# Kernel optimization log

Measured on AMD Instinct MI355X. Metric: run time of the kernel, lower is better.

Reference implementation:

```python
import jax, jax.numpy as jnp
import numpy as np

B, D, H, L = 2, 1024, 16, 4
BLK = 16                 # block_size == max_text_tokens
MT, MF = 16, 2032        # max_text_tokens, max_font_tokens
S = MT + MF              # 2048
NB = S // BLK            # 128 blocks
V = 490                  # font_vocab_size
HD = D // H              # 64
WIN = 30                 # 3*max_glyph_tokens/block_size = 3*160/16
NGLOB, NRAND = 1, 2      # BigBird global / random blocks
SOS = 0.42


def _make_layout():
    # Deterministic BigBird block layout per head: [H, NB, NB] bool
    rng = np.random.default_rng(0)
    layout = np.zeros((H, NB, NB), dtype=bool)
    layout[:, :NGLOB, :] = True          # global rows
    layout[:, :, :NGLOB] = True          # global cols
    for i in range(NB):                  # sliding window
        layout[:, i, max(0, i - WIN // 2):min(NB, i + WIN // 2 + 1)] = True
    for h in range(H):                   # random blocks
        for i in range(NB):
            layout[h, i, rng.choice(NB, size=NRAND, replace=False)] = True
    return jnp.asarray(layout)


def setup_inputs() -> dict:
    key = jax.random.key(0)
    ks = jax.random.split(key, 16)
    p = lambda k, shape: (0.02 * jax.random.normal(k, shape)).astype(jnp.float32)
    return {
        "text_embeddings": jax.random.normal(ks[0], (B, MT, D), jnp.float32),
        "font_embeddings": jax.random.normal(ks[1], (B, MF, D), jnp.float32),
        "layout": _make_layout(),
        "Wq": p(ks[2], (L, D, D)), "bq": jnp.zeros((L, D), jnp.float32),
        "Wk": p(ks[3], (L, D, D)), "bk": jnp.zeros((L, D), jnp.float32),
        "Wv": p(ks[4], (L, D, D)), "bv": jnp.zeros((L, D), jnp.float32),
        "Wo": p(ks[5], (L, D, D)), "bo": jnp.zeros((L, D), jnp.float32),
        "ln1_g": jnp.ones((L, D), jnp.float32), "ln1_b": jnp.zeros((L, D), jnp.float32),
        "ln2_g": jnp.ones((L, D), jnp.float32), "ln2_b": jnp.zeros((L, D), jnp.float32),
        "W1": p(ks[6], (L, D, 4 * D)), "b1": jnp.zeros((L, 4 * D), jnp.float32),
        "W2": p(ks[7], (L, 4 * D, D)), "b2": jnp.zeros((L, D), jnp.float32),
        "lnf_g": jnp.ones((D,), jnp.float32), "lnf_b": jnp.zeros((D,), jnp.float32),
        "Wout": p(ks[8], (D, V)),
    }


def _ln(x, g, b, eps=1e-5):
    mu = x.mean(-1, keepdims=True)
    var = ((x - mu) ** 2).mean(-1, keepdims=True)
    return (x - mu) * jax.lax.rsqrt(var + eps) * g + b


def _forward(text_embeddings, font_embeddings, layout, Wq, bq, Wk, bk, Wv, bv, Wo, bo,
             ln1_g, ln1_b, ln2_g, ln2_b, W1, b1, W2, b2, lnf_g, lnf_b, Wout):
    sos = jnp.full((B, 1, D), SOS, text_embeddings.dtype)
    x = jnp.concatenate([sos, text_embeddings, font_embeddings[:, :-1, :]], axis=1)  # [B,S,D]
    # token-level mask = block-sparse BigBird layout AND causal -> [H,S,S]
    tok_mask = jnp.repeat(jnp.repeat(layout, BLK, axis=1), BLK, axis=2)
    tok_mask = tok_mask & jnp.tril(jnp.ones((S, S), bool))[None]
    neg = jnp.asarray(-1e9, x.dtype)
    scale = jnp.asarray(1.0 / np.sqrt(HD), x.dtype)

    def layer(x, p):
        wq, bq_, wk, bk_, wv, bv_, wo, bo_, g1, gb1, g2, gb2, w1, bb1, w2, bb2 = p
        q = (x @ wq + bq_).reshape(B, S, H, HD).transpose(0, 2, 1, 3)
        k = (x @ wk + bk_).reshape(B, S, H, HD).transpose(0, 2, 1, 3)
        v = (x @ wv + bv_).reshape(B, S, H, HD).transpose(0, 2, 1, 3)
        scores = jnp.einsum('bhqd,bhkd->bhqk', q, k) * scale
        scores = jnp.where(tok_mask[None], scores, neg)
        probs = jax.nn.softmax(scores, axis=-1)
        a = jnp.einsum('bhqk,bhkd->bhqd', probs, v).transpose(0, 2, 1, 3).reshape(B, S, D)
        a = a @ wo + bo_
        x = _ln(x + a, g1, gb1)                                   # post-norm residual
        m = jax.nn.gelu(x @ w1 + bb1, approximate=False) @ w2 + bb2  # dropout=eval no-op
        x = _ln(x + m, g2, gb2)
        return x, None

    params = (Wq, bq, Wk, bk, Wv, bv, Wo, bo, ln1_g, ln1_b, ln2_g, ln2_b, W1, b1, W2, b2)
    x, _ = jax.lax.scan(jax.checkpoint(layer), x, params)
    logits = _ln(x, lnf_g, lnf_b) @ Wout                          # [B,S,V]
    return logits[:, :MT, :], logits[:, MT:, :]


def reference(text_embeddings, font_embeddings, layout, Wq, bq, Wk, bk, Wv, bv, Wo, bo,
              ln1_g, ln1_b, ln2_g, ln2_b, W1, b1, W2, b2, lnf_g, lnf_b, Wout):
    return _forward(text_embeddings, font_embeddings, layout, Wq, bq, Wk, bk, Wv, bv, Wo, bo,
                    ln1_g, ln1_b, ln2_g, ln2_b, W1, b1, W2, b2, lnf_g, lnf_b, Wout)
```

## Files before the change

kernel.cpp:

```cpp
#include <hip/hip_runtime.h>
#include <hip/hip_bf16.h>
#include <math.h>


typedef __hip_bfloat16 bf16;
typedef __attribute__((ext_vector_type(8))) short bf16x8;
typedef __attribute__((ext_vector_type(8))) unsigned short us8;
typedef __attribute__((ext_vector_type(4))) unsigned short us4;
typedef __attribute__((ext_vector_type(4))) float f32x4;
typedef __attribute__((ext_vector_type(8))) _Float16 f16x8;

#define S_LEN 2048
#define D_MODEL 1024
#define NBLK 128
#define NHEAD 16
#define BATCH 2
#define M_ROWS 4096
#define VOCAB 490

__device__ __forceinline__ float ldw(const void* p, size_t i, bool bf) {
    return bf ? __bfloat162float(((const bf16*)p)[i]) : ((const float*)p)[i];
}
__device__ __forceinline__ bool is_bf(const unsigned* probe) {
    return probe[0] != 0x3F800000u;
}
__device__ __forceinline__ unsigned short f2b(float f) {
    union { float f; unsigned u; } x; x.f = f;
    return (unsigned short)((x.u + 0x7FFFu + ((x.u >> 16) & 1u)) >> 16);
}
__device__ __forceinline__ unsigned short f2h(float f) {
    union { _Float16 h; unsigned short u; } x; x.h = (_Float16)f;
    return x.u;
}
__device__ __forceinline__ unsigned packh(float a, float b) {
    return (unsigned)f2h(a) | ((unsigned)f2h(b) << 16);
}

__global__ __launch_bounds__(256) void norm_layout_kernel(
    const unsigned char* __restrict__ lraw, unsigned char* __restrict__ mask)
{
    int i = blockIdx.x * 256 + threadIdx.x;
    bool bytes_mode = (lraw[1] == 1);
    unsigned char v;
    if (bytes_mode) v = lraw[i] ? 1 : 0;
    else            v = ((const unsigned*)lraw)[i] ? 1 : 0;
    mask[i] = v;
}

__global__ __launch_bounds__(256) void build_x_kernel(
    const void* __restrict__ text, const void* __restrict__ font,
    float* __restrict__ x, unsigned short* __restrict__ xb,
    const unsigned* __restrict__ probe)
{
    bool bf = is_bf(probe);
    size_t idx = (size_t)blockIdx.x * 256 + threadIdx.x;
    int d = (int)(idx & 1023);
    int s = (int)((idx >> 10) & 2047);
    int b = (int)(idx >> 21);
    float v;
    if (s == 0)       v = bf ? 0.419921875f : 0.42f;
    else if (s <= 16) v = ldw(text, ((size_t)(b * 16 + (s - 1))) * 1024 + d, bf);
    else              v = ldw(font, ((size_t)(b * 2032 + (s - 17))) * 1024 + d, bf);
    x[idx] = v;
    xb[idx] = f2b(v);
}

__global__ __launch_bounds__(256) void transw_kernel(
    const void* __restrict__ W, size_t wOff, unsigned short* __restrict__ Wt,
    int K, int N, const unsigned* __restrict__ probe)
{
    bool bf = is_bf(probe);
    __shared__ unsigned short tile[32][34];
    int k0 = blockIdx.x * 32, n0 = blockIdx.y * 32;
    int t = threadIdx.x, c = t & 31, r0 = t >> 5;
    #pragma unroll
    for (int i = 0; i < 4; ++i) {
        int n = n0 + c;
        float v = (n < N) ? ldw(W, wOff + (size_t)(k0 + r0 + i * 8) * N + n, bf) : 0.f;
        tile[r0 + i * 8][c] = f2b(v);
    }
    __syncthreads();
    #pragma unroll
    for (int i = 0; i < 4; ++i)
        Wt[(size_t)(n0 + r0 + i * 8) * K + k0 + c] = tile[c][r0 + i * 8];
}

__global__ __launch_bounds__(256) void transw4_kernel(
    const void* __restrict__ Wa, const void* __restrict__ Wb,
    const void* __restrict__ Wc, const void* __restrict__ Wd,
    size_t wOff, unsigned short* __restrict__ wt,
    const unsigned* __restrict__ probe)
{
    bool bf = is_bf(probe);
    int z = blockIdx.z;
    const void* W = z == 0 ? Wa : (z == 1 ? Wb : (z == 2 ? Wc : Wd));
    unsigned short* Wt = wt + (size_t)z * (1u << 20);
    __shared__ unsigned short tile[32][34];
    int k0 = blockIdx.x * 32, n0 = blockIdx.y * 32;
    int t = threadIdx.x, c = t & 31, r0 = t >> 5;
    #pragma unroll
    for (int i = 0; i < 4; ++i) {
        float v = ldw(W, wOff + (size_t)(k0 + r0 + i * 8) * 1024 + n0 + c, bf);
        tile[r0 + i * 8][c] = f2b(v);
    }
    __syncthreads();
    #pragma unroll
    for (int i = 0; i < 4; ++i)
        Wt[(size_t)(n0 + r0 + i * 8) * 1024 + k0 + c] = tile[c][r0 + i * 8];
}

__global__ __launch_bounds__(512) void gemm_kernel(
    const unsigned short* __restrict__ Ab,
    const unsigned short* __restrict__ Wt, size_t wtStride,
    const void* __restrict__ b0, const void* __restrict__ b1p, const void* __restrict__ b2p,
    size_t bOff,
    float* __restrict__ C0, float* __restrict__ C1, float* __restrict__ C2,
    void* __restrict__ Cb0, void* __restrict__ Cb1, void* __restrict__ Cb2,
    float* __restrict__ Cp,
    int M, int N, int K, int act, int outmode, const unsigned* __restrict__ probe)
{
    bool bf = is_bf(probe);
    __shared__ __align__(16) unsigned short As[2][128 * 64];
    __shared__ __align__(16) unsigned short Bs[2][128 * 64];

    int t    = threadIdx.x;
    int lane = t & 63;
    int wid  = t >> 6;
    int wm   = wid >> 2;
    int wn   = wid & 3;

    int gx  = gridDim.x;
    int nwg = gx * gridDim.y;
    int bid = blockIdx.y * gx + blockIdx.x;
    int swz = (bid & 7) * (nwg >> 3) + (bid >> 3);
    int m0  = (swz / gx) * 128;
    int n0t = (swz % gx) * 128;
    int sel = n0t / N;
    int n0  = n0t - sel * N;
    int zz  = blockIdx.z;
    int Kit = K / gridDim.z;
    int kbase = zz * Kit;

    const void* bias = sel == 0 ? b0 : (sel == 1 ? b1p : b2p);
    float* C         = sel == 0 ? C0 : (sel == 1 ? C1 : C2);
    void* Cb         = sel == 0 ? Cb0 : (sel == 1 ? Cb1 : Cb2);
    const unsigned short* Wtb = Wt + (size_t)sel * wtStride;
    const bool vtr = (outmode == 3 && sel == 2);

    f32x4 acc[4][2];
    #pragma unroll
    for (int i = 0; i < 4; i++)
        #pragma unroll
        for (int j = 0; j < 2; j++)
            acc[i][j] = (f32x4){0.f, 0.f, 0.f, 0.f};

    const int fm = lane & 15;

    auto stageA = [&](int bb, int kt) {
        int k0 = kbase + (kt << 6);
        #pragma unroll
        for (int c = 0; c < 2; ++c) {
            int p    = (wid * 2 + c) * 64 + lane;
            int row  = p >> 3;
            int cp   = p & 7;
            int csrc = cp ^ (row & 7);
            const unsigned short* src = Ab + (size_t)(m0 + row) * K + k0 + csrc * 8;
            unsigned short* dst = &As[bb][(wid * 2 + c) * 512];
            __builtin_amdgcn_global_load_lds(
                (const __attribute__((address_space(1))) unsigned int*)src,
                (__attribute__((address_space(3))) unsigned int*)dst, 16, 0, 0);
        }
    };
    auto stageB = [&](int bb, int kt) {
        int k0 = kbase + (kt << 6);
        #pragma unroll
        for (int c = 0; c < 2; ++c) {
            int p    = (wid * 2 + c) * 64 + lane;
            int row  = p >> 3;
            int cp   = p & 7;
            int csrc = cp ^ (row & 7);
            const unsigned short* src = Wtb + (size_t)(n0 + row) * K + k0 + csrc * 8;
            unsigned short* dst = &Bs[bb][(wid * 2 + c) * 512];
            __builtin_amdgcn_global_load_lds(
                (const __attribute__((address_space(1))) unsigned int*)src,
                (__attribute__((address_space(3))) unsigned int*)dst, 16, 0, 0);
        }
    };
    auto compute = [&](int bb) {
        #pragma unroll
        for (int kk = 0; kk < 2; ++kk) {
            int cq = kk * 4 + (lane >> 4);
            bf16x8 af[4], bfr[2];
            #pragma unroll
            for (int i = 0; i < 4; ++i) {
                int r = wm * 64 + i * 16 + fm;
                af[i] = *(const bf16x8*)(&As[bb][r * 64 + (cq ^ (r & 7)) * 8]);
            }
            #pragma unroll
            for (int j = 0; j < 2; ++j) {
                int n = wn * 32 + j * 16 + fm;
                bfr[j] = *(const bf16x8*)(&Bs[bb][n * 64 + (cq ^ (n & 7)) * 8]);
            }
            #pragma unroll
            for (int i = 0; i < 4; ++i)
                #pragma unroll
                for (int j = 0; j < 2; ++j)
                    acc[i][j] = __builtin_amdgcn_mfma_f32_16x16x32_bf16(
                        af[i], bfr[j], acc[i][j], 0, 0, 0);
        }
    };

    int nt = Kit >> 6;
    stageA(0, 0);
    stageB(0, 0);
    __syncthreads();

    for (int kt = 0; kt < nt; ++kt) {
        int cur = kt & 1;
        bool more = (kt + 1) < nt;
        if (more) { stageA(cur ^ 1, kt + 1); stageB(cur ^ 1, kt + 1); }
        compute(cur);
        __syncthreads();
    }

    int rq = (lane >> 4) * 4;
    #pragma unroll
    for (int j = 0; j < 2; ++j) {
        int n = n0 + wn * 32 + j * 16 + fm;
        if (n >= N) continue;
        float bv = (bias && zz == 0) ? ldw(bias, bOff + n, bf) : 0.f;
        #pragma unroll
        for (int i = 0; i < 4; ++i) {
            int mb = m0 + wm * 64 + i * 16 + rq;
            if (zz > 0) {
                #pragma unroll
                for (int r = 0; r < 4; ++r)
                    Cp[(size_t)(mb + r) * N + n] = acc[i][j][r];
                continue;
            }
            if (vtr) {
                us4 o;
                #pragma unroll
                for (int r = 0; r < 4; ++r) o[r] = f2h(acc[i][j][r] + bv);
                int bb2 = mb >> 11, s0 = mb & 2047, hh = n >> 6, dd = n & 63;
                *(us4*)(&((unsigned short*)Cb)[((((size_t)(bb2 * 16 + hh)) * 64 + dd) << 11) + s0]) = o;
                continue;
            }
            #pragma unroll
            for (int r = 0; r < 4; ++r) {
                int m = mb + r;
                float v = acc[i][j][r] + bv;
                if (act == 1) v = 0.5f * v * (1.f + erff(v * 0.70710678118654752f));
                if (outmode == 0) {
                    C[(size_t)m * N + n] = v;
                } else if (outmode == 2) {
                    ((unsigned short*)Cb)[(size_t)m * N + n] = f2b(v);
                } else if (outmode == 3) {
                    ((unsigned short*)Cb)[(size_t)m * N + n] = f2h(v);
                } else {
                    int b = m >> 11;
                    int s = m & 2047;
                    size_t dst;
                    if (s < 16) dst = ((size_t)(b * 16 + s)) * N + n;
                    else        dst = (size_t)(BATCH * 16) * N + ((size_t)(b * 2032 + (s - 16))) * N + n;
                    if (bf) ((unsigned short*)Cb)[dst] = f2b(v);
                    else    ((float*)Cb)[dst] = v;
                }
            }
        }
    }
}

__global__ __launch_bounds__(256) void attn_kernel(
    const unsigned short* __restrict__ q16, const unsigned short* __restrict__ k16,
    const unsigned short* __restrict__ v16t, const unsigned char* __restrict__ mask,
    unsigned short* __restrict__ ab)
{
    int qgrp = blockIdx.x;
    int h = blockIdx.y, b = blockIdx.z;

    __shared__ __align__(16) unsigned short ksd[64 * 64];
    __shared__ __align__(16) unsigned short vst[64 * 64];
    __shared__ unsigned char cflag[33];
    __shared__ unsigned char aclist[33];
    __shared__ int nac;

    int t = threadIdx.x, lane = t & 63, w = t >> 6;
    int qb = qgrp * 4 + w;
    const int fm = lane & 15, rq = lane >> 4;

    const unsigned char* mrow0 = mask + ((size_t)h * NBLK) * NBLK;

    if (t <= qgrp) {
        int jc = t;
        bool f = false;
        #pragma unroll
        for (int mb = 0; mb < 4; ++mb) {
            int j = jc * 4 + mb;
            #pragma unroll
            for (int ww = 0; ww < 4; ++ww) {
                int qq = qgrp * 4 + ww;
                f = f || ((j <= qq) && mrow0[qq * NBLK + j]);
            }
        }
        cflag[jc] = f ? 1 : 0;
    }
    __syncthreads();
    if (t == 0) {
        int n = 0;
        for (int jc = 0; jc <= qgrp; ++jc)
            if (cflag[jc]) aclist[n++] = (unsigned char)jc;
        nac = n;
    }

    int qrow = qb * 16 + fm;
    size_t qbase = ((size_t)(b * S_LEN + qrow)) * D_MODEL + h * 64;
    f16x8 qf0 = *(const f16x8*)(q16 + qbase + rq * 8);
    f16x8 qf1 = *(const f16x8*)(q16 + qbase + 32 + rq * 8);

    f32x4 O[4];
    #pragma unroll
    for (int c = 0; c < 4; ++c) O[c] = (f32x4){0.f, 0.f, 0.f, 0.f};
    float m_run = -1e30f, l_run = 0.f;
    const f16x8 hzero = (f16x8){0,0,0,0,0,0,0,0};

    __syncthreads();
    int nacl = nac;

    const int srow = t >> 2;
    const int sg   = (t & 3) * 2;
    const size_t vtbase = ((size_t)(b * NHEAD + h) * 64) * S_LEN;
    us8 kr0, kr1, vr0, vr1;

    auto loadKV = [&](int jc) {
        size_t kb = ((size_t)(b * S_LEN + jc * 64 + srow)) * D_MODEL + h * 64 + sg * 8;
        kr0 = *(const us8*)(k16 + kb);
        kr1 = *(const us8*)(k16 + kb + 8);
        size_t vb_ = vtbase + (size_t)srow * S_LEN + jc * 64 + sg * 8;
        vr0 = *(const us8*)(v16t + vb_);
        vr1 = *(const us8*)(v16t + vb_ + 8);
    };
    auto writeKV = [&]() {
        int p0 = (sg) ^ (srow & 7), p1 = (sg + 1) ^ (srow & 7);
        *(us8*)(&ksd[srow * 64 + p0 * 8]) = kr0;
        *(us8*)(&ksd[srow * 64 + p1 * 8]) = kr1;
        *(us8*)(&vst[srow * 64 + p0 * 8]) = vr0;
        *(us8*)(&vst[srow * 64 + p1 * 8]) = vr1;
    };

    if (nacl > 0) loadKV(aclist[0]);

    for (int ci = 0; ci < nacl; ++ci) {
        int jc = aclist[ci];
        __syncthreads();
        writeKV();
        if (ci + 1 < nacl) loadKV(aclist[ci + 1]);
        __syncthreads();

        #pragma unroll
        for (int mb = 0; mb < 4; ++mb) {
            int j = jc * 4 + mb;
            bool actv = (j <= qb) && mrow0[qb * NBLK + j];
            if (!actv) continue;

            int krow = mb * 16 + fm;
            f16x8 kf0 = *(const f16x8*)(&ksd[krow * 64 + ((0 * 4 + rq) ^ (krow & 7)) * 8]);
            f16x8 kf1 = *(const f16x8*)(&ksd[krow * 64 + ((1 * 4 + rq) ^ (krow & 7)) * 8]);
            f32x4 st = (f32x4){0.f, 0.f, 0.f, 0.f};
            st = __builtin_amdgcn_mfma_f32_16x16x32_f16(kf0, qf0, st, 0, 0, 0);
            st = __builtin_amdgcn_mfma_f32_16x16x32_f16(kf1, qf1, st, 0, 0, 0);

            float s[4];
            #pragma unroll
            for (int r = 0; r < 4; ++r) {
                s[r] = st[r] * 0.125f;
                if (j == qb && (rq * 4 + r) > fm) s[r] = -1e30f;
            }
            float mx = fmaxf(fmaxf(s[0], s[1]), fmaxf(s[2], s[3]));
            mx = fmaxf(mx, __shfl_xor(mx, 16));
            mx = fmaxf(mx, __shfl_xor(mx, 32));
            mx = fmaxf(m_run, mx);
            float al = expf(m_run - mx);
            float p[4]; float ls = 0.f;
            #pragma unroll
            for (int r = 0; r < 4; ++r) {
                p[r] = (s[r] < -1e29f) ? 0.f : expf(s[r] - mx);
                ls += p[r];
            }
            ls += __shfl_xor(ls, 16);
            ls += __shfl_xor(ls, 32);
            l_run = l_run * al + ls;
            m_run = mx;

            unsigned ph01 = packh(p[0], p[1]), ph23 = packh(p[2], p[3]);
            int s0 = fm + (((rq & 1) * 2) << 4);
            int s1 = s0 + 16;
            unsigned w0 = __shfl(ph01, s0), w1 = __shfl(ph23, s0);
            unsigned w2 = __shfl(ph01, s1), w3 = __shfl(ph23, s1);
            union { unsigned u[4]; f16x8 v; } pcv;
            pcv.u[0] = w0; pcv.u[1] = w1; pcv.u[2] = w2; pcv.u[3] = w3;
            f16x8 pa = (rq < 2) ? pcv.v : hzero;

            float al0 = __shfl(al, rq * 4 + 0), al1 = __shfl(al, rq * 4 + 1);
            float al2 = __shfl(al, rq * 4 + 2), al3 = __shfl(al, rq * 4 + 3);
            #pragma unroll
            for (int c = 0; c < 4; ++c) {
                O[c][0] *= al0; O[c][1] *= al1; O[c][2] *= al2; O[c][3] *= al3;
                f16x8 vb = hzero;
                if (rq < 2) {
                    int vrow = c * 16 + fm;
                    vb = *(const f16x8*)(&vst[vrow * 64 + ((mb * 2 + rq) ^ (vrow & 7)) * 8]);
                }
                O[c] = __builtin_amdgcn_mfma_f32_16x16x32_f16(pa, vb, O[c], 0, 0, 0);
            }
        }
    }

    float li0 = 1.f / __shfl(l_run, rq * 4 + 0);
    float li1 = 1.f / __shfl(l_run, rq * 4 + 1);
    float li2 = 1.f / __shfl(l_run, rq * 4 + 2);
    float li3 = 1.f / __shfl(l_run, rq * 4 + 3);
    size_t obase = ((size_t)(b * S_LEN + qb * 16)) * D_MODEL + h * 64;
    #pragma unroll
    for (int c = 0; c < 4; ++c) {
        ab[obase + (size_t)(rq * 4 + 0) * D_MODEL + c * 16 + fm] = f2b(O[c][0] * li0);
        ab[obase + (size_t)(rq * 4 + 1) * D_MODEL + c * 16 + fm] = f2b(O[c][1] * li1);
        ab[obase + (size_t)(rq * 4 + 2) * D_MODEL + c * 16 + fm] = f2b(O[c][2] * li2);
        ab[obase + (size_t)(rq * 4 + 3) * D_MODEL + c * 16 + fm] = f2b(O[c][3] * li3);
    }
}

__global__ __launch_bounds__(256) void add_ln_kernel(
    const float* __restrict__ xin, const float* __restrict__ res,
    const float* __restrict__ res2,
    float* __restrict__ xout, unsigned short* __restrict__ bfout,
    const void* __restrict__ g, size_t gOff,
    const void* __restrict__ bt, size_t bOff, const unsigned* __restrict__ probe)
{
    bool bf = is_bf(probe);
    int row = blockIdx.x;
    int t = threadIdx.x;
    __shared__ float red[4];

    float4 xv = ((const float4*)(xin + (size_t)row * D_MODEL))[t];
    if (res) {
        float4 rv = ((const float4*)(res + (size_t)row * D_MODEL))[t];
        xv.x += rv.x; xv.y += rv.y; xv.z += rv.z; xv.w += rv.w;
    }
    if (res2) {
        float4 rv = ((const float4*)(res2 + (size_t)row * D_MODEL))[t];
        xv.x += rv.x; xv.y += rv.y; xv.z += rv.z; xv.w += rv.w;
    }
    float s = xv.x + xv.y + xv.z + xv.w;
    for (int off = 32; off > 0; off >>= 1) s += __shfl_down(s, off);
    if ((t & 63) == 0) red[t >> 6] = s;
    __syncthreads();
    float mu = (red[0] + red[1] + red[2] + red[3]) * (1.f / 1024.f);
    __syncthreads();

    float d0 = xv.x - mu, d1 = xv.y - mu, d2 = xv.z - mu, d3 = xv.w - mu;
    float s2 = d0 * d0 + d1 * d1 + d2 * d2 + d3 * d3;
    for (int off = 32; off > 0; off >>= 1) s2 += __shfl_down(s2, off);
    if ((t & 63) == 0) red[t >> 6] = s2;
    __syncthreads();
    float var = (red[0] + red[1] + red[2] + red[3]) * (1.f / 1024.f);
    float rstd = rsqrtf(var + 1e-5f);

    int dbase = t * 4;
    float4 ov;
    ov.x = d0 * rstd * ldw(g, gOff + dbase + 0, bf) + ldw(bt, bOff + dbase + 0, bf);
    ov.y = d1 * rstd * ldw(g, gOff + dbase + 1, bf) + ldw(bt, bOff + dbase + 1, bf);
    ov.z = d2 * rstd * ldw(g, gOff + dbase + 2, bf) + ldw(bt, bOff + dbase + 2, bf);
    ov.w = d3 * rstd * ldw(g, gOff + dbase + 3, bf) + ldw(bt, bOff + dbase + 3, bf);
    ((float4*)(xout + (size_t)row * D_MODEL))[t] = ov;
    if (bfout) {
        us4 bv = { f2b(ov.x), f2b(ov.y), f2b(ov.z), f2b(ov.w) };
        *(us4*)(bfout + (size_t)row * D_MODEL + dbase) = bv;
    }
}

extern "C" void kernel_launch(void* const* d_in, const int* in_sizes, int n_in,
                              void* d_out, int out_size, void* d_ws, size_t ws_size,
                              hipStream_t stream) {
    const void* text  = d_in[0];
    const void* font  = d_in[1];
    const unsigned char* lraw = (const unsigned char*)d_in[2];
    const void* Wq    = d_in[3];
    const void* bq    = d_in[4];
    const void* Wk    = d_in[5];
    const void* bk    = d_in[6];
    const void* Wv    = d_in[7];
    const void* bv    = d_in[8];
    const void* Wo    = d_in[9];
    const void* bo_   = d_in[10];
    const void* ln1g  = d_in[11];
    const void* ln1b  = d_in[12];
    const void* ln2g  = d_in[13];
    const void* ln2b  = d_in[14];
    const void* W1    = d_in[15];
    const void* b1    = d_in[16];
    const void* W2    = d_in[17];
    const void* b2    = d_in[18];
    const void* lnfg  = d_in[19];
    const void* lnfb  = d_in[20];
    const void* Wout  = d_in[21];
    const unsigned* probe = (const unsigned*)d_in[11];

    const size_t Q = (size_t)M_ROWS * D_MODEL;
    float* ws = (float*)d_ws;
    float* x  = ws;
    float* G0 = ws + Q;
    unsigned short* q16 = (unsigned short*)(ws + 2 * Q);
    unsigned short* k16 = q16 + Q;
    unsigned short* v16 = k16 + Q;
    unsigned short* hb  = (unsigned short*)(ws + 2 * Q);
    unsigned short* xb  = (unsigned short*)(ws + 4 * Q);
    unsigned short* ab  = (unsigned short*)(ws + 4 * Q + Q / 2);
    unsigned char* mask = (unsigned char*)(ws + 5 * Q);
    unsigned short* wt  = (unsigned short*)((char*)d_ws + 5 * Q * 4 + 262144);

    const size_t baseEnd = 5 * Q * 4 + 262144 + 8 * ((size_t)1 << 20) * 2;
    bool canSplit = ws_size >= baseEnd + Q * 4;
    float* part = (float*)((char*)d_ws + baseEnd);

    norm_layout_kernel<<<(NHEAD * NBLK * NBLK) / 256, 256, 0, stream>>>(lraw, mask);
    build_x_kernel<<<(BATCH * S_LEN * D_MODEL) / 256, 256, 0, stream>>>(text, font, x, xb, probe);

    dim3 gQKV(3 * D_MODEL / 128, M_ROWS / 128);
    dim3 gD(D_MODEL / 128, M_ROWS / 128, canSplit ? 2 : 1);
    dim3 gF(4 * D_MODEL / 128, M_ROWS / 128);
    dim3 gV((VOCAB + 127) / 128, M_ROWS / 128);

    const size_t MSZ = (size_t)1 << 20;
    const float* r2 = canSplit ? part : nullptr;

    for (int l = 0; l < 4; l++) {
        size_t wo  = (size_t)l * D_MODEL * D_MODEL;
        size_t bo1 = (size_t)l * D_MODEL;
        size_t w1o = (size_t)l * D_MODEL * 4 * D_MODEL;
        size_t b1o = (size_t)l * 4 * D_MODEL;

        transw4_kernel<<<dim3(32, 32, 4), 256, 0, stream>>>(Wq, Wk, Wv, Wo, wo, wt, probe);

        gemm_kernel<<<gQKV, 512, 0, stream>>>(xb, wt, MSZ, bq, bk, bv, bo1,
                                              nullptr, nullptr, nullptr, q16, k16, v16,
                                              nullptr,
                                              M_ROWS, D_MODEL, D_MODEL, 0, 3, probe);
        attn_kernel<<<dim3(S_LEN / 64, NHEAD, BATCH), 256, 0, stream>>>(
            q16, k16, v16, mask, ab);
        gemm_kernel<<<gD, 512, 0, stream>>>(ab, wt + 3 * MSZ, 0, bo_, bo_, bo_, bo1,
                                            G0, G0, G0, nullptr, nullptr, nullptr,
                                            part,
                                            M_ROWS, D_MODEL, D_MODEL, 0, 0, probe);
        add_ln_kernel<<<M_ROWS, 256, 0, stream>>>(x, G0, r2, x, xb, ln1g, bo1, ln1b, bo1, probe);

        transw_kernel<<<dim3(32, 128), 256, 0, stream>>>(W1, w1o, wt, D_MODEL, 4 * D_MODEL, probe);
        transw_kernel<<<dim3(128, 32), 256, 0, stream>>>(W2, w1o, wt + 4 * MSZ, 4 * D_MODEL, D_MODEL, probe);

        gemm_kernel<<<gF, 512, 0, stream>>>(xb, wt, 0, b1, b1, b1, b1o,
                                            nullptr, nullptr, nullptr, hb, hb, hb,
                                            nullptr,
                                            M_ROWS, 4 * D_MODEL, D_MODEL, 1, 2, probe);
        gemm_kernel<<<gD, 512, 0, stream>>>(hb, wt + 4 * MSZ, 0, b2, b2, b2, bo1,
                                            G0, G0, G0, nullptr, nullptr, nullptr,
                                            part,
                                            M_ROWS, D_MODEL, 4 * D_MODEL, 0, 0, probe);
        add_ln_kernel<<<M_ROWS, 256, 0, stream>>>(x, G0, r2, x, xb, ln2g, bo1, ln2b, bo1, probe);
    }

    add_ln_kernel<<<M_ROWS, 256, 0, stream>>>(x, nullptr, nullptr, G0, ab, lnfg, 0, lnfb, 0, probe);
    transw_kernel<<<dim3(32, 16), 256, 0, stream>>>(Wout, 0, wt, D_MODEL, VOCAB, probe);
    gemm_kernel<<<gV, 512, 0, stream>>>(ab, wt, 0, nullptr, nullptr, nullptr, 0,
                                        nullptr, nullptr, nullptr, d_out, d_out, d_out,
                                        nullptr,
                                        M_ROWS, VOCAB, D_MODEL, 0, 1, probe);
}
```

Measured before the change: 1.332 ms.

## Vectorize weight transposes, use polynomial GELU, reverse attention block order

The weight transpose kernels now read and write four elements per thread with vector loads and stores, and the shared tile is padded to 36 columns. The exact erff in the GELU epilogue is replaced by an Abramowitz-Stegun polynomial using a fast reciprocal and __expf, which lowers accuracy to about 1e-7 absolute error in erf. The attention grid processes query groups in reverse order so the heavier late blocks with more active key columns are scheduled first. These are separate ideas that each target conversion bandwidth, epilogue math cost, or load balance.

Measured after the change: 1.309 ms. Within noise of the previous version (-1.7%).

```diff
diff --git a/kernel.cpp b/kernel.cpp
--- a/kernel.cpp
+++ b/kernel.cpp
@@ -34,6 +34,15 @@
 }
 __device__ __forceinline__ unsigned packh(float a, float b) {
     return (unsigned)f2h(a) | ((unsigned)f2h(b) << 16);
+}
+__device__ __forceinline__ float gelu_exact(float v) {
+    float z = fabsf(v) * 0.70710678118654752f;
+    float t = __builtin_amdgcn_rcpf(fmaf(0.3275911f, z, 1.f));
+    float p = t * fmaf(t, fmaf(t, fmaf(t, fmaf(t, 1.061405429f, -1.453152027f),
+                  1.421413741f), -0.284496736f), 0.254829592f);
+    float er = 1.f - p * __expf(-z * z);
+    er = copysignf(er, v);
+    return 0.5f * v * (1.f + er);
 }
 
 __global__ __launch_bounds__(256) void norm_layout_kernel(
@@ -70,19 +79,32 @@
     int K, int N, const unsigned* __restrict__ probe)
 {
     bool bf = is_bf(probe);
-    __shared__ unsigned short tile[32][34];
+    __shared__ unsigned short tile[32][36];
     int k0 = blockIdx.x * 32, n0 = blockIdx.y * 32;
-    int t = threadIdx.x, c = t & 31, r0 = t >> 5;
-    #pragma unroll
-    for (int i = 0; i < 4; ++i) {
-        int n = n0 + c;
-        float v = (n < N) ? ldw(W, wOff + (size_t)(k0 + r0 + i * 8) * N + n, bf) : 0.f;
-        tile[r0 + i * 8][c] = f2b(v);
-    }
-    __syncthreads();
-    #pragma unroll
-    for (int i = 0; i < 4; ++i)
-        Wt[(size_t)(n0 + r0 + i * 8) * K + k0 + c] = tile[c][r0 + i * 8];
+    int t = threadIdx.x;
+    int r  = t >> 3;
+    int c4 = (t & 7) * 4;
+    int n = n0 + c4;
+    us4 tv;
+    if (n + 4 <= N) {
+        if (bf) {
+            tv = *(const us4*)((const unsigned short*)W + wOff + (size_t)(k0 + r) * N + n);
+        } else {
+            float4 f = *(const float4*)((const float*)W + wOff + (size_t)(k0 + r) * N + n);
+            tv = (us4){ f2b(f.x), f2b(f.y), f2b(f.z), f2b(f.w) };
+        }
+    } else {
+        #pragma unroll
+        for (int i = 0; i < 4; ++i)
+            tv[i] = (n + i < N) ? f2b(ldw(W, wOff + (size_t)(k0 + r) * N + n + i, bf))
+                                : (unsigned short)0;
+    }
+    *(us4*)(&tile[r][c4]) = tv;
+    __syncthreads();
+    int rn = t >> 3;
+    int k4 = (t & 7) * 4;
+    us4 ov = { tile[k4 + 0][rn], tile[k4 + 1][rn], tile[k4 + 2][rn], tile[k4 + 3][rn] };
+    *(us4*)(&Wt[(size_t)(n0 + rn) * K + k0 + k4]) = ov;
 }
 
 __global__ __launch_bounds__(256) void transw4_kernel(
@@ -95,18 +117,24 @@
     int z = blockIdx.z;
     const void* W = z == 0 ? Wa : (z == 1 ? Wb : (z == 2 ? Wc : Wd));
     unsigned short* Wt = wt + (size_t)z * (1u << 20);
-    __shared__ unsigned short tile[32][34];
+    __shared__ unsigned short tile[32][36];
     int k0 = blockIdx.x * 32, n0 = blockIdx.y * 32;
-    int t = threadIdx.x, c = t & 31, r0 = t >> 5;
-    #pragma unroll
-    for (int i = 0; i < 4; ++i) {
-        float v = ldw(W, wOff + (size_t)(k0 + r0 + i * 8) * 1024 + n0 + c, bf);
-        tile[r0 + i * 8][c] = f2b(v);
-    }
-    __syncthreads();
-    #pragma unroll
-    for (int i = 0; i < 4; ++i)
-        Wt[(size_t)(n0 + r0 + i * 8) * 1024 + k0 + c] = tile[c][r0 + i * 8];
+    int t = threadIdx.x;
+    int r  = t >> 3;
+    int c4 = (t & 7) * 4;
+    us4 tv;
+    if (bf) {
+        tv = *(const us4*)((const unsigned short*)W + wOff + (size_t)(k0 + r) * 1024 + n0 + c4);
+    } else {
+        float4 f = *(const float4*)((const float*)W + wOff + (size_t)(k0 + r) * 1024 + n0 + c4);
+        tv = (us4){ f2b(f.x), f2b(f.y), f2b(f.z), f2b(f.w) };
+    }
+    *(us4*)(&tile[r][c4]) = tv;
+    __syncthreads();
+    int rn = t >> 3;
+    int k4 = (t & 7) * 4;
+    us4 ov = { tile[k4 + 0][rn], tile[k4 + 1][rn], tile[k4 + 2][rn], tile[k4 + 3][rn] };
+    *(us4*)(&Wt[(size_t)(n0 + rn) * 1024 + k0 + k4]) = ov;
 }
 
 __global__ __launch_bounds__(512) void gemm_kernel(
@@ -250,7 +278,7 @@
             for (int r = 0; r < 4; ++r) {
                 int m = mb + r;
                 float v = acc[i][j][r] + bv;
-                if (act == 1) v = 0.5f * v * (1.f + erff(v * 0.70710678118654752f));
+                if (act == 1) v = gelu_exact(v);
                 if (outmode == 0) {
                     C[(size_t)m * N + n] = v;
                 } else if (outmode == 2) {
@@ -276,7 +304,7 @@
     const unsigned short* __restrict__ v16t, const unsigned char* __restrict__ mask,
     unsigned short* __restrict__ ab)
 {
-    int qgrp = blockIdx.x;
+    int qgrp = (S_LEN / 64 - 1) - blockIdx.x;
     int h = blockIdx.y, b = blockIdx.z;
 
     __shared__ __align__(16) unsigned short ksd[64 * 64];
```
